# Performance work log

Measured on AMD Instinct MI355X. Metric: run time of the kernel, lower is better.

The kernel has to match this reference:

```python
import jax, jax.numpy as jnp
import numpy as np

N_NODES = 100000
N_EDGES = 1600000
IN_CH = 128
HID = 128
EMBED = 256
NUM_GRAPHS = 128


def setup_inputs() -> dict:
    key = jax.random.key(0)
    ks = jax.random.split(key, 12)
    x = jax.random.normal(ks[0], (N_NODES, IN_CH), dtype=jnp.float32)
    edge_index = jax.random.randint(ks[1], (2, N_EDGES), 0, N_NODES, dtype=jnp.int64)
    batch = jnp.sort(jax.random.randint(ks[2], (N_NODES,), 0, NUM_GRAPHS, dtype=jnp.int64))
    s = 0.05
    # conv1 MLP: Linear(in_ch,128) -> ReLU -> Linear(128,128)
    W11 = jax.random.normal(ks[3], (IN_CH, HID), dtype=jnp.float32) * s
    b11 = jnp.zeros((HID,), dtype=jnp.float32)
    W12 = jax.random.normal(ks[4], (HID, HID), dtype=jnp.float32) * s
    b12 = jnp.zeros((HID,), dtype=jnp.float32)
    # conv2 MLP: Linear(128,128) -> ReLU -> Linear(128,embed)
    W21 = jax.random.normal(ks[5], (HID, HID), dtype=jnp.float32) * s
    b21 = jnp.zeros((HID,), dtype=jnp.float32)
    W22 = jax.random.normal(ks[6], (HID, EMBED), dtype=jnp.float32) * s
    b22 = jnp.zeros((EMBED,), dtype=jnp.float32)
    gamma = jnp.ones((EMBED,), dtype=jnp.float32)
    beta = jnp.zeros((EMBED,), dtype=jnp.float32)
    return {"x": x, "edge_index": edge_index, "batch": batch,
            "W11": W11, "b11": b11, "W12": W12, "b12": b12,
            "W21": W21, "b21": b21, "W22": W22, "b22": b22,
            "gamma": gamma, "beta": beta}


def _gin_conv(x, src, dst, W_a, b_a, W_b, b_b):
    # GINConv with eps=0: MLP(x + sum_{j in N(i)} x_j)
    msgs = x[src]                                   # [E, d] gather
    agg = jax.ops.segment_sum(msgs, dst, num_segments=N_NODES)  # scatter-add
    h = x + agg
    h = jax.nn.relu(h @ W_a + b_a)
    return h @ W_b + b_b


def reference(x, edge_index, batch, W11, b11, W12, b12, W21, b21, W22, b22, gamma, beta):
    src, dst = edge_index[0], edge_index[1]
    h = jax.nn.relu(_gin_conv(x, src, dst, W11, b11, W12, b12))   # [N, 128]
    h = jax.nn.relu(_gin_conv(h, src, dst, W21, b21, W22, b22))   # [N, 256]
    # global_mean_pool over graphs
    sums = jax.ops.segment_sum(h, batch, num_segments=NUM_GRAPHS)           # [G, 256]
    counts = jax.ops.segment_sum(jnp.ones((N_NODES,), h.dtype), batch, num_segments=NUM_GRAPHS)
    pooled = sums / jnp.maximum(counts, 1.0)[:, None]
    # LayerNorm over last dim (eps=1e-5 as in torch)
    mu = jnp.mean(pooled, axis=-1, keepdims=True)
    var = jnp.var(pooled, axis=-1, keepdims=True)
    out = (pooled - mu) * jax.lax.rsqrt(var + 1e-5) * gamma + beta
    # Dropout in eval mode: identity
    return out
```

## Files before the change

### kernel.cpp

```cpp
#include <hip/hip_runtime.h>

#define GRAPHS 128
#define CHUNKC 8000

typedef _Float16 f16x8 __attribute__((ext_vector_type(8)));
typedef _Float16 f16x4 __attribute__((ext_vector_type(4)));
typedef _Float16 f16x2 __attribute__((ext_vector_type(2)));
typedef float f32x4 __attribute__((ext_vector_type(4)));

__global__ void k_hist(const int* __restrict__ dst, int* __restrict__ histG,
                       int e, int NB, int NW) {
  __shared__ int h[256];
  int t = threadIdx.x, w = blockIdx.x;
  h[t] = 0; __syncthreads();
  int lo = w * CHUNKC, hi = min(lo + CHUNKC, e);
  for (int i = lo + t; i < hi; i += 256) atomicAdd(&h[dst[i] >> 9], 1);
  __syncthreads();
  if (t < NB) histG[t * NW + w] = h[t];
}

__global__ void k_scanA(const int* __restrict__ in, int* __restrict__ out,
                        int* __restrict__ bsum, int N) {
  __shared__ int s[256];
  int t = threadIdx.x, b = blockIdx.x;
  int base = b * 1024 + t * 4;
  int v[4]; int tot = 0;
#pragma unroll
  for (int j = 0; j < 4; ++j) { int i = base + j; v[j] = (i < N) ? in[i] : 0; tot += v[j]; }
  s[t] = tot; __syncthreads();
  for (int o = 1; o < 256; o <<= 1) {
    int x = (t >= o) ? s[t - o] : 0;
    __syncthreads(); s[t] += x; __syncthreads();
  }
  int run = s[t] - tot;
#pragma unroll
  for (int j = 0; j < 4; ++j) { int i = base + j; if (i < N) out[i] = run; run += v[j]; }
  if (t == 255) bsum[b] = s[255];
}

__global__ void k_scanB(int* bsum, int nb) {
  __shared__ int s[256];
  int t = threadIdx.x;
  int v = (t < nb) ? bsum[t] : 0;
  s[t] = v; __syncthreads();
  for (int o = 1; o < 256; o <<= 1) {
    int x = (t >= o) ? s[t - o] : 0;
    __syncthreads(); s[t] += x; __syncthreads();
  }
  if (t < nb) bsum[t] = s[t] - v;
}

__global__ void k_scanC(int* __restrict__ out, const int* __restrict__ bsum, int N) {
  int i = blockIdx.x * 256 + threadIdx.x;
  if (i < N) out[i] += bsum[i >> 10];
}

__global__ void k_part(const int* __restrict__ src, const int* __restrict__ dst,
                       const int* __restrict__ histG, const int* __restrict__ off,
                       int* __restrict__ part, int e, int NB, int NW) {
  __shared__ int hist[256], lbA[256], lbB[256], stmp[256];
  __shared__ int els[CHUNKC];
  int t = threadIdx.x, w = blockIdx.x;
  int hv = (t < NB) ? histG[t * NW + w] : 0;
  hist[t] = hv; stmp[t] = hv; __syncthreads();
  for (int o = 1; o < 256; o <<= 1) {
    int x = (t >= o) ? stmp[t - o] : 0;
    __syncthreads(); stmp[t] += x; __syncthreads();
  }
  lbA[t] = stmp[t] - hv; lbB[t] = stmp[t] - hv;
  __syncthreads();
  int lo = w * CHUNKC, hi = min(lo + CHUNKC, e);
  for (int i = lo + t; i < hi; i += 256) {
    int d = dst[i];
    int p = atomicAdd(&lbB[d >> 9], 1);
    els[p] = src[i] | ((d & 511) << 17);
  }
  __syncthreads();
  int ln = t & 63, wv = t >> 6;
  for (int b = wv; b < NB; b += 4) {
    int c = hist[b], lb = lbA[b];
    long g = off[b * NW + w];
    for (int j = ln; j < c; j += 64) part[g + j] = els[lb + j];
  }
}

__global__ void k_csrb(const int* __restrict__ part, const int* __restrict__ off,
                       int* __restrict__ ptr, int* __restrict__ csr,
                       int e, int NB, int NW, int n) {
  __shared__ int nh[512], ncur[512], stmp[256];
  int t = threadIdx.x, b = blockIdx.x;
  int s0 = off[b * NW];
  int e0 = (b + 1 < NB) ? off[(b + 1) * NW] : e;
  nh[t] = 0; nh[t + 256] = 0; __syncthreads();
  for (int i = s0 + t; i < e0; i += 256) atomicAdd(&nh[((unsigned)part[i]) >> 17], 1);
  __syncthreads();
  int v0 = nh[2 * t], v1 = nh[2 * t + 1];
  int ps = v0 + v1;
  stmp[t] = ps; __syncthreads();
  for (int o = 1; o < 256; o <<= 1) {
    int x = (t >= o) ? stmp[t - o] : 0;
    __syncthreads(); stmp[t] += x; __syncthreads();
  }
  int base = stmp[t] - ps;
  __syncthreads();
  nh[2 * t] = base;   nh[2 * t + 1] = base + v0;
  ncur[2 * t] = base; ncur[2 * t + 1] = base + v0;
  __syncthreads();
#pragma unroll
  for (int q = 0; q < 2; ++q) {
    int vv = t + q * 256;
    int node = (b << 9) + vv;
    if (node <= n) ptr[node] = s0 + nh[vv];
  }
  for (int i = s0 + t; i < e0; i += 256) {
    int u = part[i];
    int p = atomicAdd(&ncur[((unsigned)u) >> 17], 1);
    csr[s0 + p] = u & 0x1FFFF;
  }
}

__global__ void k_cvt(const float* __restrict__ in, _Float16* __restrict__ out, int total4) {
  int i = blockIdx.x * 256 + threadIdx.x;
  if (i >= total4) return;
  float4 v = ((const float4*)in)[i];
  f16x4 h = { (_Float16)v.x, (_Float16)v.y, (_Float16)v.z, (_Float16)v.w };
  ((f16x4*)out)[i] = h;
}

__global__ void k_agg_h(const _Float16* __restrict__ in, _Float16* __restrict__ out,
                        const int* __restrict__ ptr, const int* __restrict__ csr, int n) {
  int gid = blockIdx.x * 256 + threadIdx.x;
  int node = gid >> 6, lane = gid & 63;
  if (node >= n) return;
  const f16x8* inp = (const f16x8*)in;
  int cb = lane & 15, rg = lane >> 4;
  f16x8 self = inp[(size_t)node * 16 + cb];
  float acc[8];
#pragma unroll
  for (int c = 0; c < 8; ++c) acc[c] = (rg == 0) ? (float)self[c] : 0.f;
  int s = ptr[node], deg = ptr[node + 1] - s;
  for (int seg = 0; seg < deg; seg += 64) {
    int my = (seg + lane < deg) ? csr[s + seg + lane] : n;
    int segn = min(deg - seg, 64);
    for (int b2 = 0; b2 < segn; b2 += 32) {
      int jj[8]; f16x8 w[8];
#pragma unroll
      for (int u = 0; u < 8; ++u) jj[u] = __shfl(my, b2 + u * 4 + rg);
#pragma unroll
      for (int u = 0; u < 8; ++u) w[u] = inp[(size_t)jj[u] * 16 + cb];
#pragma unroll
      for (int u = 0; u < 8; ++u)
#pragma unroll
        for (int c = 0; c < 8; ++c) acc[c] += (float)w[u][c];
    }
  }
#pragma unroll
  for (int c = 0; c < 8; ++c) {
    acc[c] += __shfl_xor(acc[c], 16);
    acc[c] += __shfl_xor(acc[c], 32);
  }
  if (rg == 0) {
    f16x8 r;
#pragma unroll
    for (int c = 0; c < 8; ++c) r[c] = (_Float16)acc[c];
    ((f16x8*)out)[(size_t)node * 16 + cb] = r;
  }
}

__global__ void k_wprep_all(const float* __restrict__ W11, const float* __restrict__ W12,
                            const float* __restrict__ W21, const float* __restrict__ W22,
                            _Float16* __restrict__ w11t, _Float16* __restrict__ w12t,
                            _Float16* __restrict__ w21t, _Float16* __restrict__ w22t) {
  int b = blockIdx.x, k = threadIdx.x;
  const float* W; _Float16* Wt; int c, C;
  if (b < 128)      { W = W11; Wt = w11t; c = b;       C = 128; }
  else if (b < 256) { W = W12; Wt = w12t; c = b - 128; C = 128; }
  else if (b < 384) { W = W21; Wt = w21t; c = b - 256; C = 128; }
  else              { W = W22; Wt = w22t; c = b - 384; C = 256; }
  Wt[c * 128 + k] = (_Float16)W[k * C + c];
}

__launch_bounds__(512)
__global__ void k_mlp128(const _Float16* __restrict__ in, const _Float16* __restrict__ WtA,
                         const float* __restrict__ bA, const _Float16* __restrict__ WtB,
                         const float* __restrict__ bB, _Float16* __restrict__ out, int n) {
  __shared__ _Float16 xs[256 * 136];
  __shared__ _Float16 wa[128 * 136];
  __shared__ _Float16 wb[128 * 136];
  int t = threadIdx.x;
  int r0 = blockIdx.x * 256;
#pragma unroll
  for (int i = 0; i < 8; ++i) {
    int id = t + i * 512;
    int row = id >> 4, k8 = id & 15;
    f16x8 v = {0, 0, 0, 0, 0, 0, 0, 0};
    if (r0 + row < n) v = ((const f16x8*)in)[(size_t)(r0 + row) * 16 + k8];
    *(f16x8*)&xs[row * 136 + k8 * 8] = v;
  }
#pragma unroll
  for (int i = 0; i < 4; ++i) {
    int id = t + i * 512;
    int c = id >> 4, k8 = id & 15;
    *(f16x8*)&wa[c * 136 + k8 * 8] = ((const f16x8*)WtA)[c * 16 + k8];
    *(f16x8*)&wb[c * 136 + k8 * 8] = ((const f16x8*)WtB)[c * 16 + k8];
  }
  __syncthreads();
  int lane = t & 63, w = t >> 6;
  int l16 = lane & 15, lk = (lane >> 4) * 8;
  int rw = w * 32;
  int rloc = rw + (lane >> 4) * 4;
  f32x4 acc[2][8];
#pragma unroll
  for (int fr = 0; fr < 2; ++fr)
#pragma unroll
    for (int fc = 0; fc < 8; ++fc) acc[fr][fc] = (f32x4){0.f, 0.f, 0.f, 0.f};
#pragma unroll
  for (int kk = 0; kk < 4; ++kk) {
    int klo = kk * 32 + lk;
    f16x8 a0 = *(const f16x8*)&xs[(rw + l16) * 136 + klo];
    f16x8 a1 = *(const f16x8*)&xs[(rw + 16 + l16) * 136 + klo];
#pragma unroll
    for (int fc = 0; fc < 8; ++fc) {
      f16x8 b = *(const f16x8*)&wa[(fc * 16 + l16) * 136 + klo];
      acc[0][fc] = __builtin_amdgcn_mfma_f32_16x16x32_f16(a0, b, acc[0][fc], 0, 0, 0);
      acc[1][fc] = __builtin_amdgcn_mfma_f32_16x16x32_f16(a1, b, acc[1][fc], 0, 0, 0);
    }
  }
#pragma unroll
  for (int fr = 0; fr < 2; ++fr)
#pragma unroll
    for (int fc = 0; fc < 8; ++fc) {
      int col = fc * 16 + l16;
      float bv = bA[col];
#pragma unroll
      for (int j = 0; j < 4; ++j)
        xs[(rloc + fr * 16 + j) * 136 + col] = (_Float16)fmaxf(acc[fr][fc][j] + bv, 0.f);
    }
#pragma unroll
  for (int fr = 0; fr < 2; ++fr)
#pragma unroll
    for (int fc = 0; fc < 8; ++fc) acc[fr][fc] = (f32x4){0.f, 0.f, 0.f, 0.f};
#pragma unroll
  for (int kk = 0; kk < 4; ++kk) {
    int klo = kk * 32 + lk;
    f16x8 a0 = *(const f16x8*)&xs[(rw + l16) * 136 + klo];
    f16x8 a1 = *(const f16x8*)&xs[(rw + 16 + l16) * 136 + klo];
#pragma unroll
    for (int fc = 0; fc < 8; ++fc) {
      f16x8 b = *(const f16x8*)&wb[(fc * 16 + l16) * 136 + klo];
      acc[0][fc] = __builtin_amdgcn_mfma_f32_16x16x32_f16(a0, b, acc[0][fc], 0, 0, 0);
      acc[1][fc] = __builtin_amdgcn_mfma_f32_16x16x32_f16(a1, b, acc[1][fc], 0, 0, 0);
    }
  }
#pragma unroll
  for (int fr = 0; fr < 2; ++fr)
#pragma unroll
    for (int fc = 0; fc < 8; ++fc) {
      int col = fc * 16 + l16;
      float bv = bB[col];
#pragma unroll
      for (int j = 0; j < 4; ++j) {
        int row = r0 + rloc + fr * 16 + j;
        if (row < n) out[(size_t)row * 128 + col] = (_Float16)fmaxf(acc[fr][fc][j] + bv, 0.f);
      }
    }
}

__launch_bounds__(512)
__global__ void k_mlp_pool(const _Float16* __restrict__ in, const _Float16* __restrict__ WtA,
                           const float* __restrict__ bA, const _Float16* __restrict__ WtB,
                           const float* __restrict__ bB, const int* __restrict__ batch,
                           float* __restrict__ pool, int n) {
  __shared__ _Float16 xs[256 * 136];
  __shared__ _Float16 wa[128 * 136];
  __shared__ _Float16 wb[128 * 136];
  __shared__ float pool_l[8 * 256];
  int t = threadIdx.x;
  int r0 = blockIdx.x * 256;
#pragma unroll
  for (int j = 0; j < 4; ++j) pool_l[j * 512 + t] = 0.f;
#pragma unroll
  for (int i = 0; i < 8; ++i) {
    int id = t + i * 512;
    int row = id >> 4, k8 = id & 15;
    f16x8 v = {0, 0, 0, 0, 0, 0, 0, 0};
    if (r0 + row < n) v = ((const f16x8*)in)[(size_t)(r0 + row) * 16 + k8];
    *(f16x8*)&xs[row * 136 + k8 * 8] = v;
  }
#pragma unroll
  for (int i = 0; i < 4; ++i) {
    int id = t + i * 512;
    int c = id >> 4, k8 = id & 15;
    *(f16x8*)&wa[c * 136 + k8 * 8] = ((const f16x8*)WtA)[c * 16 + k8];
    *(f16x8*)&wb[c * 136 + k8 * 8] = ((const f16x8*)WtB)[c * 16 + k8];
  }
  __syncthreads();
  int lane = t & 63, w = t >> 6;
  int l16 = lane & 15, lk = (lane >> 4) * 8;
  int rw = w * 32;
  int rloc = rw + (lane >> 4) * 4;
  int g0 = batch[r0];
  int g4[2][4];
#pragma unroll
  for (int fr = 0; fr < 2; ++fr)
#pragma unroll
    for (int j = 0; j < 4; ++j) {
      int row = r0 + rloc + fr * 16 + j;
      g4[fr][j] = (row < n) ? batch[row] : -1;
    }
  f32x4 acc[2][8];
#pragma unroll
  for (int fr = 0; fr < 2; ++fr)
#pragma unroll
    for (int fc = 0; fc < 8; ++fc) acc[fr][fc] = (f32x4){0.f, 0.f, 0.f, 0.f};
#pragma unroll
  for (int kk = 0; kk < 4; ++kk) {
    int klo = kk * 32 + lk;
    f16x8 a0 = *(const f16x8*)&xs[(rw + l16) * 136 + klo];
    f16x8 a1 = *(const f16x8*)&xs[(rw + 16 + l16) * 136 + klo];
#pragma unroll
    for (int fc = 0; fc < 8; ++fc) {
      f16x8 b = *(const f16x8*)&wa[(fc * 16 + l16) * 136 + klo];
      acc[0][fc] = __builtin_amdgcn_mfma_f32_16x16x32_f16(a0, b, acc[0][fc], 0, 0, 0);
      acc[1][fc] = __builtin_amdgcn_mfma_f32_16x16x32_f16(a1, b, acc[1][fc], 0, 0, 0);
    }
  }
#pragma unroll
  for (int fr = 0; fr < 2; ++fr)
#pragma unroll
    for (int fc = 0; fc < 8; ++fc) {
      int col = fc * 16 + l16;
      float bv = bA[col];
#pragma unroll
      for (int j = 0; j < 4; ++j)
        xs[(rloc + fr * 16 + j) * 136 + col] = (_Float16)fmaxf(acc[fr][fc][j] + bv, 0.f);
    }
  for (int h = 0; h < 2; ++h) {
    if (h) {
      __syncthreads();
#pragma unroll
      for (int i = 0; i < 4; ++i) {
        int id = t + i * 512;
        int c = id >> 4, k8 = id & 15;
        *(f16x8*)&wb[c * 136 + k8 * 8] = ((const f16x8*)WtB)[(128 + c) * 16 + k8];
      }
      __syncthreads();
    }
#pragma unroll
    for (int fr = 0; fr < 2; ++fr)
#pragma unroll
      for (int fc = 0; fc < 8; ++fc) acc[fr][fc] = (f32x4){0.f, 0.f, 0.f, 0.f};
#pragma unroll
    for (int kk = 0; kk < 4; ++kk) {
      int klo = kk * 32 + lk;
      f16x8 a0 = *(const f16x8*)&xs[(rw + l16) * 136 + klo];
      f16x8 a1 = *(const f16x8*)&xs[(rw + 16 + l16) * 136 + klo];
#pragma unroll
      for (int fc = 0; fc < 8; ++fc) {
        f16x8 b = *(const f16x8*)&wb[(fc * 16 + l16) * 136 + klo];
        acc[0][fc] = __builtin_amdgcn_mfma_f32_16x16x32_f16(a0, b, acc[0][fc], 0, 0, 0);
        acc[1][fc] = __builtin_amdgcn_mfma_f32_16x16x32_f16(a1, b, acc[1][fc], 0, 0, 0);
      }
    }
#pragma unroll
    for (int fc = 0; fc < 8; ++fc) {
      int col = h * 128 + fc * 16 + l16;
      float bv = bB[col];
#pragma unroll
      for (int fr = 0; fr < 2; ++fr) {
        f32x4 a = acc[fr][fc];
        float run = fmaxf(a[0] + bv, 0.f);
#pragma unroll
        for (int j = 1; j < 4; ++j) {
          float v = fmaxf(a[j] + bv, 0.f);
          if (g4[fr][j] == g4[fr][j - 1]) run += v;
          else {
            int g = g4[fr][j - 1];
            if (g >= 0) {
              int d = g - g0;
              if (d >= 0 && d < 8) atomicAdd(&pool_l[d * 256 + col], run);
              else atomicAdd(&pool[g * 256 + col], run);
            }
            run = v;
          }
        }
        int g = g4[fr][3];
        if (g >= 0) {
          int d = g - g0;
          if (d >= 0 && d < 8) atomicAdd(&pool_l[d * 256 + col], run);
          else atomicAdd(&pool[g * 256 + col], run);
        }
      }
    }
  }
  __syncthreads();
#pragma unroll
  for (int j = 0; j < 4; ++j) {
    int idx = j * 512 + t;
    int g = g0 + (idx >> 8), col = idx & 255;
    float v = pool_l[idx];
    if (g < GRAPHS && v != 0.f) atomicAdd(&pool[g * 256 + col], v);
  }
}

__global__ void k_starts(const int* __restrict__ batch, int* __restrict__ starts, int n) {
  int g = threadIdx.x;
  if (g > GRAPHS) return;
  int lo = 0, hi = n;
  while (lo < hi) { int mid = (lo + hi) >> 1; if (batch[mid] < g) lo = mid + 1; else hi = mid; }
  starts[g] = lo;
}

__global__ void k_final(const float* __restrict__ pool, const int* __restrict__ starts,
                        const float* __restrict__ gamma, const float* __restrict__ beta,
                        float* __restrict__ out) {
  __shared__ float2 red[256];
  int g = blockIdx.x, ch = threadIdx.x;
  int cnt = starts[g + 1] - starts[g];
  float p = pool[g * 256 + ch] / fmaxf((float)cnt, 1.f);
  red[ch] = make_float2(p, p * p);
  __syncthreads();
  for (int off = 128; off > 0; off >>= 1) {
    if (ch < off) { red[ch].x += red[ch + off].x; red[ch].y += red[ch + off].y; }
    __syncthreads();
  }
  float mu = red[0].x * (1.f / 256.f);
  float var = red[0].y * (1.f / 256.f) - mu * mu;
  out[g * 256 + ch] = (p - mu) * rsqrtf(var + 1e-5f) * gamma[ch] + beta[ch];
}

extern "C" void kernel_launch(void* const* d_in, const int* in_sizes, int n_in,
                              void* d_out, int out_size, void* d_ws, size_t ws_size,
                              hipStream_t stream) {
  const float* x     = (const float*)d_in[0];
  const int*   ei    = (const int*)d_in[1];
  const int*   batch = (const int*)d_in[2];
  const float* W11 = (const float*)d_in[3];  const float* b11 = (const float*)d_in[4];
  const float* W12 = (const float*)d_in[5];  const float* b12 = (const float*)d_in[6];
  const float* W21 = (const float*)d_in[7];  const float* b21 = (const float*)d_in[8];
  const float* W22 = (const float*)d_in[9];  const float* b22 = (const float*)d_in[10];
  const float* gamma = (const float*)d_in[11];
  const float* beta  = (const float*)d_in[12];
  float* out = (float*)d_out;

  int n = in_sizes[0] / 128;
  int e = in_sizes[1] / 2;
  const int* src = ei;
  const int* dstv = ei + e;

  int NB = (n + 511) >> 9;
  int NW = (e + CHUNKC - 1) / CHUNKC;
  int NS = NB * NW;

  char* ws = (char*)d_ws;
  auto alloc = [&](size_t bytes) { char* p = ws; ws += (bytes + 15) & ~(size_t)15; return p; };
  _Float16* P0 = (_Float16*)alloc((size_t)(n + 1) * 128 * 2);
  _Float16* P1 = (_Float16*)alloc((size_t)(n + 1) * 128 * 2);
  float* pool  = (float*)alloc((size_t)GRAPHS * 256 * 4);
  int* ptr     = (int*)alloc((size_t)(n + 1) * 4);
  int* csr     = (int*)alloc((size_t)e * 4);
  int* part    = (int*)alloc((size_t)e * 4);
  int* histG   = (int*)alloc((size_t)NS * 4);
  int* off     = (int*)alloc((size_t)NS * 4);
  int* bsum    = (int*)alloc(256 * 4);
  int* starts  = (int*)alloc((GRAPHS + 1) * 4);
  _Float16* w11t = (_Float16*)alloc(128 * 128 * 2);
  _Float16* w12t = (_Float16*)alloc(128 * 128 * 2);
  _Float16* w21t = (_Float16*)alloc(128 * 128 * 2);
  _Float16* w22t = (_Float16*)alloc(256 * 128 * 2);

  hipMemsetAsync(pool, 0, (size_t)GRAPHS * 256 * 4, stream);
  hipMemsetAsync(P0 + (size_t)n * 128, 0, 256, stream);

  int nbk = (NS + 1023) / 1024;
  k_hist <<<NW, 256, 0, stream>>>(dstv, histG, e, NB, NW);
  k_scanA<<<nbk, 256, 0, stream>>>(histG, off, bsum, NS);
  k_scanB<<<1, 256, 0, stream>>>(bsum, nbk);
  k_scanC<<<(NS + 255) / 256, 256, 0, stream>>>(off, bsum, NS);
  k_part <<<NW, 256, 0, stream>>>(src, dstv, histG, off, part, e, NB, NW);
  k_csrb <<<NB, 256, 0, stream>>>(part, off, ptr, csr, e, NB, NW, n);
  k_starts<<<1, 256, 0, stream>>>(batch, starts, n);
  k_wprep_all<<<640, 128, 0, stream>>>(W11, W12, W21, W22, w11t, w12t, w21t, w22t);
  k_cvt<<<(n * 32 + 255) / 256, 256, 0, stream>>>(x, P0, n * 32);

  int mb = (n + 255) / 256;
  int ab = (n * 64 + 255) / 256;

  k_agg_h<<<ab, 256, 0, stream>>>(P0, P1, ptr, csr, n);
  k_mlp128<<<mb, 512, 0, stream>>>(P1, w11t, b11, w12t, b12, P0, n);
  k_agg_h<<<ab, 256, 0, stream>>>(P0, P1, ptr, csr, n);
  k_mlp_pool<<<mb, 512, 0, stream>>>(P1, w21t, b21, w22t, b22, batch, pool, n);
  k_final<<<GRAPHS, 256, 0, stream>>>(pool, starts, gamma, beta, out);
}
```

Baseline: 317.7 us.

## Load MLP operands directly from global memory and shrink tiles to 128 rows

Result: slower. 365.7 us (+15.1%).

```diff
diff --git a/kernel.cpp b/kernel.cpp
--- a/kernel.cpp
+++ b/kernel.cpp
@@ -180,35 +180,21 @@
   Wt[c * 128 + k] = (_Float16)W[k * C + c];
 }
 
-__launch_bounds__(512)
+__launch_bounds__(256)
 __global__ void k_mlp128(const _Float16* __restrict__ in, const _Float16* __restrict__ WtA,
                          const float* __restrict__ bA, const _Float16* __restrict__ WtB,
                          const float* __restrict__ bB, _Float16* __restrict__ out, int n) {
-  __shared__ _Float16 xs[256 * 136];
-  __shared__ _Float16 wa[128 * 136];
-  __shared__ _Float16 wb[128 * 136];
+  __shared__ _Float16 hs[128 * 136];
   int t = threadIdx.x;
-  int r0 = blockIdx.x * 256;
-#pragma unroll
-  for (int i = 0; i < 8; ++i) {
-    int id = t + i * 512;
-    int row = id >> 4, k8 = id & 15;
-    f16x8 v = {0, 0, 0, 0, 0, 0, 0, 0};
-    if (r0 + row < n) v = ((const f16x8*)in)[(size_t)(r0 + row) * 16 + k8];
-    *(f16x8*)&xs[row * 136 + k8 * 8] = v;
-  }
-#pragma unroll
-  for (int i = 0; i < 4; ++i) {
-    int id = t + i * 512;
-    int c = id >> 4, k8 = id & 15;
-    *(f16x8*)&wa[c * 136 + k8 * 8] = ((const f16x8*)WtA)[c * 16 + k8];
-    *(f16x8*)&wb[c * 136 + k8 * 8] = ((const f16x8*)WtB)[c * 16 + k8];
-  }
-  __syncthreads();
+  int r0 = blockIdx.x * 128;
   int lane = t & 63, w = t >> 6;
-  int l16 = lane & 15, lk = (lane >> 4) * 8;
+  int l16 = lane & 15, rg = lane >> 4;
   int rw = w * 32;
-  int rloc = rw + (lane >> 4) * 4;
+  const f16x8* inp = (const f16x8*)in;
+  const f16x8* wa = (const f16x8*)WtA;
+  const f16x8* wb = (const f16x8*)WtB;
+  int ra0 = r0 + rw + l16;       if (ra0 > n) ra0 = n;
+  int ra1 = r0 + rw + 16 + l16;  if (ra1 > n) ra1 = n;
   f32x4 acc[2][8];
 #pragma unroll
   for (int fr = 0; fr < 2; ++fr)
@@ -216,89 +202,78 @@
     for (int fc = 0; fc < 8; ++fc) acc[fr][fc] = (f32x4){0.f, 0.f, 0.f, 0.f};
 #pragma unroll
   for (int kk = 0; kk < 4; ++kk) {
-    int klo = kk * 32 + lk;
-    f16x8 a0 = *(const f16x8*)&xs[(rw + l16) * 136 + klo];
-    f16x8 a1 = *(const f16x8*)&xs[(rw + 16 + l16) * 136 + klo];
+    int ck = kk * 4 + rg;
+    f16x8 a0 = inp[(size_t)ra0 * 16 + ck];
+    f16x8 a1 = inp[(size_t)ra1 * 16 + ck];
 #pragma unroll
     for (int fc = 0; fc < 8; ++fc) {
-      f16x8 b = *(const f16x8*)&wa[(fc * 16 + l16) * 136 + klo];
+      f16x8 b = wa[(fc * 16 + l16) * 16 + ck];
       acc[0][fc] = __builtin_amdgcn_mfma_f32_16x16x32_f16(a0, b, acc[0][fc], 0, 0, 0);
       acc[1][fc] = __builtin_amdgcn_mfma_f32_16x16x32_f16(a1, b, acc[1][fc], 0, 0, 0);
     }
   }
+  int rloc = rw + rg * 4;
+#pragma unroll
+  for (int fc = 0; fc < 8; ++fc) {
+    int col = fc * 16 + l16;
+    float bv = bA[col];
+#pragma unroll
+    for (int fr = 0; fr < 2; ++fr)
+#pragma unroll
+      for (int j = 0; j < 4; ++j)
+        hs[(rloc + fr * 16 + j) * 136 + col] = (_Float16)fmaxf(acc[fr][fc][j] + bv, 0.f);
+  }
 #pragma unroll
   for (int fr = 0; fr < 2; ++fr)
 #pragma unroll
+    for (int fc = 0; fc < 8; ++fc) acc[fr][fc] = (f32x4){0.f, 0.f, 0.f, 0.f};
+#pragma unroll
+  for (int kk = 0; kk < 4; ++kk) {
+    int klo = kk * 32 + rg * 8;
+    f16x8 a0 = *(const f16x8*)&hs[(rw + l16) * 136 + klo];
+    f16x8 a1 = *(const f16x8*)&hs[(rw + 16 + l16) * 136 + klo];
+#pragma unroll
     for (int fc = 0; fc < 8; ++fc) {
-      int col = fc * 16 + l16;
-      float bv = bA[col];
-#pragma unroll
-      for (int j = 0; j < 4; ++j)
-        xs[(rloc + fr * 16 + j) * 136 + col] = (_Float16)fmaxf(acc[fr][fc][j] + bv, 0.f);
-    }
-#pragma unroll
-  for (int fr = 0; fr < 2; ++fr)
-#pragma unroll
-    for (int fc = 0; fc < 8; ++fc) acc[fr][fc] = (f32x4){0.f, 0.f, 0.f, 0.f};
-#pragma unroll
-  for (int kk = 0; kk < 4; ++kk) {
-    int klo = kk * 32 + lk;
-    f16x8 a0 = *(const f16x8*)&xs[(rw + l16) * 136 + klo];
-    f16x8 a1 = *(const f16x8*)&xs[(rw + 16 + l16) * 136 + klo];
-#pragma unroll
-    for (int fc = 0; fc < 8; ++fc) {
-      f16x8 b = *(const f16x8*)&wb[(fc * 16 + l16) * 136 + klo];
+      f16x8 b = wb[(fc * 16 + l16) * 16 + kk * 4 + rg];
       acc[0][fc] = __builtin_amdgcn_mfma_f32_16x16x32_f16(a0, b, acc[0][fc], 0, 0, 0);
       acc[1][fc] = __builtin_amdgcn_mfma_f32_16x16x32_f16(a1, b, acc[1][fc], 0, 0, 0);
     }
   }
 #pragma unroll
-  for (int fr = 0; fr < 2; ++fr)
-#pragma unroll
-    for (int fc = 0; fc < 8; ++fc) {
-      int col = fc * 16 + l16;
-      float bv = bB[col];
+  for (int fc = 0; fc < 8; ++fc) {
+    int col = fc * 16 + l16;
+    float bv = bB[col];
+#pragma unroll
+    for (int fr = 0; fr < 2; ++fr)
 #pragma unroll
       for (int j = 0; j < 4; ++j) {
         int row = r0 + rloc + fr * 16 + j;
         if (row < n) out[(size_t)row * 128 + col] = (_Float16)fmaxf(acc[fr][fc][j] + bv, 0.f);
       }
-    }
-}
-
-__launch_bounds__(512)
+  }
+}
+
+__launch_bounds__(256)
 __global__ void k_mlp_pool(const _Float16* __restrict__ in, const _Float16* __restrict__ WtA,
                            const float* __restrict__ bA, const _Float16* __restrict__ WtB,
                            const float* __restrict__ bB, const int* __restrict__ batch,
                            float* __restrict__ pool, int n) {
-  __shared__ _Float16 xs[256 * 136];
-  __shared__ _Float16 wa[128 * 136];
-  __shared__ _Float16 wb[128 * 136];
+  __shared__ _Float16 hs[128 * 136];
   __shared__ float pool_l[8 * 256];
   int t = threadIdx.x;
-  int r0 = blockIdx.x * 256;
-#pragma unroll
-  for (int j = 0; j < 4; ++j) pool_l[j * 512 + t] = 0.f;
-#pragma unroll
-  for (int i = 0; i < 8; ++i) {
-    int id = t + i * 512;
-    int row = id >> 4, k8 = id & 15;
-    f16x8 v = {0, 0, 0, 0, 0, 0, 0, 0};
-    if (r0 + row < n) v = ((const f16x8*)in)[(size_t)(r0 + row) * 16 + k8];
-    *(f16x8*)&xs[row * 136 + k8 * 8] = v;
-  }
-#pragma unroll
-  for (int i = 0; i < 4; ++i) {
-    int id = t + i * 512;
-    int c = id >> 4, k8 = id & 15;
-    *(f16x8*)&wa[c * 136 + k8 * 8] = ((const f16x8*)WtA)[c * 16 + k8];
-    *(f16x8*)&wb[c * 136 + k8 * 8] = ((const f16x8*)WtB)[c * 16 + k8];
-  }
+  int r0 = blockIdx.x * 128;
+#pragma unroll
+  for (int j = 0; j < 8; ++j) pool_l[j * 256 + t] = 0.f;
   __syncthreads();
   int lane = t & 63, w = t >> 6;
-  int l16 = lane & 15, lk = (lane >> 4) * 8;
+  int l16 = lane & 15, rg = lane >> 4;
   int rw = w * 32;
-  int rloc = rw + (lane >> 4) * 4;
+  const f16x8* inp = (const f16x8*)in;
+  const f16x8* wa = (const f16x8*)WtA;
+  const f16x8* wb = (const f16x8*)WtB;
+  int ra0 = r0 + rw + l16;       if (ra0 > n) ra0 = n;
+  int ra1 = r0 + rw + 16 + l16;  if (ra1 > n) ra1 = n;
+  int rloc = rw + rg * 4;
   int g0 = batch[r0];
   int g4[2][4];
 #pragma unroll
@@ -315,49 +290,39 @@
     for (int fc = 0; fc < 8; ++fc) acc[fr][fc] = (f32x4){0.f, 0.f, 0.f, 0.f};
 #pragma unroll
   for (int kk = 0; kk < 4; ++kk) {
-    int klo = kk * 32 + lk;
-    f16x8 a0 = *(const f16x8*)&xs[(rw + l16) * 136 + klo];
-    f16x8 a1 = *(const f16x8*)&xs[(rw + 16 + l16) * 136 + klo];
+    int ck = kk * 4 + rg;
+    f16x8 a0 = inp[(size_t)ra0 * 16 + ck];
+    f16x8 a1 = inp[(size_t)ra1 * 16 + ck];
 #pragma unroll
     for (int fc = 0; fc < 8; ++fc) {
-      f16x8 b = *(const f16x8*)&wa[(fc * 16 + l16) * 136 + klo];
+      f16x8 b = wa[(fc * 16 + l16) * 16 + ck];
       acc[0][fc] = __builtin_amdgcn_mfma_f32_16x16x32_f16(a0, b, acc[0][fc], 0, 0, 0);
       acc[1][fc] = __builtin_amdgcn_mfma_f32_16x16x32_f16(a1, b, acc[1][fc], 0, 0, 0);
     }
   }
 #pragma unroll
-  for (int fr = 0; fr < 2; ++fr)
-#pragma unroll
-    for (int fc = 0; fc < 8; ++fc) {
-      int col = fc * 16 + l16;
-      float bv = bA[col];
+  for (int fc = 0; fc < 8; ++fc) {
+    int col = fc * 16 + l16;
+    float bv = bA[col];
+#pragma unroll
+    for (int fr = 0; fr < 2; ++fr)
 #pragma unroll
       for (int j = 0; j < 4; ++j)
-        xs[(rloc + fr * 16 + j) * 136 + col] = (_Float16)fmaxf(acc[fr][fc][j] + bv, 0.f);
-    }
+        hs[(rloc + fr * 16 + j) * 136 + col] = (_Float16)fmaxf(acc[fr][fc][j] + bv, 0.f);
+  }
   for (int h = 0; h < 2; ++h) {
-    if (h) {
-      __syncthreads();
-#pragma unroll
-      for (int i = 0; i < 4; ++i) {
-        int id = t + i * 512;
-        int c = id >> 4, k8 = id & 15;
-        *(f16x8*)&wb[c * 136 + k8 * 8] = ((const f16x8*)WtB)[(128 + c) * 16 + k8];
-      }
-      __syncthreads();
-    }
 #pragma unroll
     for (int fr = 0; fr < 2; ++fr)
 #pragma unroll
       for (int fc = 0; fc < 8; ++fc) acc[fr][fc] = (f32x4){0.f, 0.f, 0.f, 0.f};
 #pragma unroll
     for (int kk = 0; kk < 4; ++kk) {
-      int klo = kk * 32 + lk;
-      f16x8 a0 = *(const f16x8*)&xs[(rw + l16) * 136 + klo];
-      f16x8 a1 = *(const f16x8*)&xs[(rw + 16 + l16) * 136 + klo];
+      int klo = kk * 32 + rg * 8;
+      f16x8 a0 = *(const f16x8*)&hs[(rw + l16) * 136 + klo];
+      f16x8 a1 = *(const f16x8*)&hs[(rw + 16 + l16) * 136 + klo];
 #pragma unroll
       for (int fc = 0; fc < 8; ++fc) {
-        f16x8 b = *(const f16x8*)&wb[(fc * 16 + l16) * 136 + klo];
+        f16x8 b = wb[(h * 128 + fc * 16 + l16) * 16 + kk * 4 + rg];
         acc[0][fc] = __builtin_amdgcn_mfma_f32_16x16x32_f16(a0, b, acc[0][fc], 0, 0, 0);
         acc[1][fc] = __builtin_amdgcn_mfma_f32_16x16x32_f16(a1, b, acc[1][fc], 0, 0, 0);
       }
@@ -395,8 +360,8 @@
   }
   __syncthreads();
 #pragma unroll
-  for (int j = 0; j < 4; ++j) {
-    int idx = j * 512 + t;
+  for (int j = 0; j < 8; ++j) {
+    int idx = j * 256 + t;
     int g = g0 + (idx >> 8), col = idx & 255;
     float v = pool_l[idx];
     if (g < GRAPHS && v != 0.f) atomicAdd(&pool[g * 256 + col], v);
@@ -471,6 +436,7 @@
 
   hipMemsetAsync(pool, 0, (size_t)GRAPHS * 256 * 4, stream);
   hipMemsetAsync(P0 + (size_t)n * 128, 0, 256, stream);
+  hipMemsetAsync(P1 + (size_t)n * 128, 0, 256, stream);
 
   int nbk = (NS + 1023) / 1024;
   k_hist <<<NW, 256, 0, stream>>>(dstv, histG, e, NB, NW);
@@ -483,12 +449,12 @@
   k_wprep_all<<<640, 128, 0, stream>>>(W11, W12, W21, W22, w11t, w12t, w21t, w22t);
   k_cvt<<<(n * 32 + 255) / 256, 256, 0, stream>>>(x, P0, n * 32);
 
-  int mb = (n + 255) / 256;
+  int mb = (n + 127) / 128;
   int ab = (n * 64 + 255) / 256;
 
   k_agg_h<<<ab, 256, 0, stream>>>(P0, P1, ptr, csr, n);
-  k_mlp128<<<mb, 512, 0, stream>>>(P1, w11t, b11, w12t, b12, P0, n);
+  k_mlp128<<<mb, 256, 0, stream>>>(P1, w11t, b11, w12t, b12, P0, n);
   k_agg_h<<<ab, 256, 0, stream>>>(P0, P1, ptr, csr, n);
-  k_mlp_pool<<<mb, 512, 0, stream>>>(P1, w21t, b21, w22t, b22, batch, pool, n);
+  k_mlp_pool<<<mb, 256, 0, stream>>>(P1, w21t, b21, w22t, b22, batch, pool, n);
   k_final<<<GRAPHS, 256, 0, stream>>>(pool, starts, gamma, beta, out);
 }
```
